# Performance work log

Hardware: AMD Instinct MI355X
Metric: run time of the kernel (lower is better)

## Reference

```python
import jax, jax.numpy as jnp
import numpy as np

DECAY_INIT = 0.9
SPECTRAL_RADIUS = 0.5
EPS = 1e-8


def _spectral_normed(W, u, radius):
    # 3 power iterations (no-grad in torch); u, v treated as constants.
    for _ in range(3):
        v = W.T @ u
        v = v / (jnp.linalg.norm(v) + EPS)
        u = W @ v
        u = u / (jnp.linalg.norm(u) + EPS)
    u = jax.lax.stop_gradient(u)
    v = jax.lax.stop_gradient(v)
    sigma = jnp.abs(u @ W @ v)
    return W * (radius / (sigma + EPS))


def setup_inputs() -> dict:
    key = jax.random.key(0)
    ks = jax.random.split(key, 6)
    T, B, D, n = 2048, 8, 1024, 64
    xavier = float(np.sqrt(2.0 / (D + n)))
    x = jax.random.normal(ks[0], (T, B, D), dtype=jnp.float32)
    S0 = jnp.zeros((B, n, n), dtype=jnp.float32)
    W_k = jax.random.normal(ks[1], (n, D), dtype=jnp.float32) * xavier
    W_v = jax.random.normal(ks[2], (n, D), dtype=jnp.float32) * xavier
    W_q = jax.random.normal(ks[3], (n, D), dtype=jnp.float32) * xavier
    u_k = jax.random.normal(ks[4], (n,), dtype=jnp.float32)
    u_k = u_k / (jnp.linalg.norm(u_k) + EPS)
    u_v = jax.random.normal(ks[5], (n,), dtype=jnp.float32)
    u_v = u_v / (jnp.linalg.norm(u_v) + EPS)
    return {"x": x, "S0": S0, "W_k": W_k, "W_v": W_v, "W_q": W_q,
            "u_k": u_k, "u_v": u_v}


def reference(x, S0, W_k, W_v, W_q, u_k, u_v):
    # decay = clamp(0.9, 0, 0.999).item() -> detached constant
    decay = jnp.clip(jnp.float32(DECAY_INIT), 0.0, 0.999)
    Wk = _spectral_normed(W_k, u_k, SPECTRAL_RADIUS)
    Wv = _spectral_normed(W_v, u_v, SPECTRAL_RADIUS)

    # projections: [T, B, n]
    k_all = jnp.einsum('tbd,nd->tbn', x, Wk)
    v_all = jnp.einsum('tbd,nd->tbn', x, Wv)
    q_all = jnp.einsum('tbd,nd->tbn', x, W_q)

    def step(S, kvq):
        k, v, q = kvq  # each [B, n]
        S = decay * S + v[:, :, None] * k[:, None, :]  # [B, n, n]
        sq = jnp.einsum('bij,bj->bi', S, q)
        out = sq * jax.nn.silu(sq)
        return S, (S, out)

    _, (S_seq, output) = jax.lax.scan(step, S0, (k_all, v_all, q_all))
    S_all = jnp.concatenate([S0[None], S_seq], axis=0)  # [T+1, B, n, n]
    return output, S_all
```

## Files before the change

kernel.cpp:

```cpp
#include <hip/hip_runtime.h>
#include <math.h>

#define T_DIM 2048
#define B_DIM 8
#define D_DIM 1024
#define N_DIM 64
#define NCHUNK 16
#define CHUNK_LEN 128
#define DECAY 0.9f
#define EPS 1e-8f
#define RADIUS 0.5f

typedef __attribute__((ext_vector_type(8))) short short8;
typedef __attribute__((ext_vector_type(4))) float f32x4;

static __device__ __forceinline__ unsigned short f2bf(float f) {
    unsigned u = __float_as_uint(f);
    u += 0x7FFFu + ((u >> 16) & 1u);
    return (unsigned short)(u >> 16);
}
static __device__ __forceinline__ float bf2f(unsigned short h) {
    return __uint_as_float(((unsigned)h) << 16);
}

static __device__ __forceinline__ void bar_lgkm() {
    asm volatile("s_waitcnt lgkmcnt(0)" ::: "memory");
    __builtin_amdgcn_s_barrier();
    asm volatile("" ::: "memory");
}

__global__ __launch_bounds__(256)
void gram_kernel(const float* __restrict__ Wk, const float* __restrict__ Wv,
                 float* __restrict__ G) {
    int mat = blockIdx.x >> 6;
    int i   = blockIdx.x & 63;
    const float* W = mat ? Wv : Wk;
    __shared__ float wsr[D_DIM];
    __shared__ float part[4][64];
    int tid = threadIdx.x;
    *(float4*)&wsr[tid * 4] = *(const float4*)(W + (size_t)i * D_DIM + tid * 4);
    __syncthreads();
    int j = tid & 63, p = tid >> 6;
    const float* wj = W + (size_t)j * D_DIM + p * 256;
    const float* wp = wsr + p * 256;
    float acc = 0.f;
    #pragma unroll 16
    for (int k = 0; k < 256; k += 4) {
        float4 a = *(const float4*)(wj + k);
        float4 b = *(const float4*)(wp + k);
        acc += a.x * b.x + a.y * b.y + a.z * b.z + a.w * b.w;
    }
    part[p][j] = acc;
    __syncthreads();
    if (tid < 64)
        G[((size_t)mat * 64 + i) * 64 + tid] =
            part[0][tid] + part[1][tid] + part[2][tid] + part[3][tid];
}

__global__ __launch_bounds__(256)
void build_wt_kernel(const float* __restrict__ Wk, const float* __restrict__ Wv,
                     const float* __restrict__ Wq, const float* __restrict__ G,
                     const float* __restrict__ uk, const float* __restrict__ uv,
                     unsigned short* __restrict__ BPh, unsigned short* __restrict__ BPl) {
    __shared__ float Gs[64][65];
    __shared__ float us_s[64];
    __shared__ float sc_s;
    int bid = blockIdx.x;
    int g   = bid >> 3;
    int gm  = g >> 2;
    int tid = threadIdx.x;

    if (gm < 2) {
        #pragma unroll
        for (int e = 0; e < 16; ++e) {
            int idx = e * 256 + tid;
            Gs[idx >> 6][idx & 63] = G[(size_t)gm * 4096 + idx];
        }
        if (tid < 64) us_s[tid] = (gm ? uv : uk)[tid];
        __syncthreads();
        if (tid < 64) {
            int i = tid;
            float sigma = 0.f;
            for (int it = 0; it < 3; ++it) {
                float t = 0.f;
                #pragma unroll
                for (int jj = 0; jj < 64; ++jj)
                    t += Gs[i][jj] * us_s[jj];
                float nv2 = us_s[i] * t;
                #pragma unroll
                for (int o = 32; o > 0; o >>= 1) nv2 += __shfl_xor(nv2, o, 64);
                float nv = sqrtf(fmaxf(nv2, 0.f));
                float ur = t / (nv + EPS);
                float nu2 = ur * ur;
                #pragma unroll
                for (int o = 32; o > 0; o >>= 1) nu2 += __shfl_xor(nu2, o, 64);
                float nu = sqrtf(nu2);
                if (it == 2) sigma = nu2 / (nu + EPS);
                us_s[i] = ur / (nu + EPS);
            }
            if (tid == 0) sc_s = RADIUS / (sigma + EPS);
        }
    } else {
        if (tid == 0) sc_s = 1.0f;
    }
    __syncthreads();
    float sc = sc_s;

    const float* W = (gm == 0) ? Wk : (gm == 1) ? Wv : Wq;
    int subb = bid & 7;
    int m    = subb * 256 + tid;
    int s    = m >> 7;
    int kk   = (m >> 6) & 1;
    int flh  = (m >> 4) & 3;
    int fl   = m & 15;
    int row  = (g & 3) * 16 + fl;
    int k0   = s * 64 + kk * 32 + flh * 8;
    const float* src = W + (size_t)row * D_DIM + k0;
    float4 a = *(const float4*)src;
    float4 b = *(const float4*)(src + 4);
    float v[8] = {a.x, a.y, a.z, a.w, b.x, b.y, b.z, b.w};
    short8 hv, lv;
    #pragma unroll
    for (int e = 0; e < 8; ++e) {
        float val = v[e] * sc;
        unsigned short hh = f2bf(val);
        hv[e] = (short)hh;
        lv[e] = (short)f2bf(val - bf2f(hh));
    }
    size_t o = (size_t)g * 16384 + (size_t)m * 8;
    *(short8*)(BPh + o) = hv;
    *(short8*)(BPl + o) = lv;
}

#define PBM 32
#define KSTAGE 128
__global__ __launch_bounds__(256)
void proj_mfma_kernel(const float* __restrict__ x,
                      const unsigned short* __restrict__ BPh,
                      const unsigned short* __restrict__ BPl,
                      float* __restrict__ kvq) {
    __shared__ __align__(16) unsigned short ldsA[2][PBM * KSTAGE];
    int tid = threadIdx.x;
    int lane = tid & 63;
    int wv = tid >> 6;
    int fl15 = lane & 15;
    int flh = lane >> 4;
    int rowBase = blockIdx.x * PBM;

    int r_st = tid >> 3;
    int sub  = tid & 7;
    const float* xrow = x + (size_t)(rowBase + r_st) * D_DIM + sub * 8;
    int wb0 = r_st * 256 + ((sub * 16) ^ ((r_st & 7) << 4));
    int wb1 = wb0 + 128;

    const unsigned short* bbh = BPh + (size_t)(wv * 3) * 16384 + lane * 8;
    const unsigned short* bbl = BPl + (size_t)(wv * 3) * 16384 + lane * 8;

    f32x4 acc[2][3];
    #pragma unroll
    for (int mt = 0; mt < 2; ++mt)
        #pragma unroll
        for (int nt = 0; nt < 3; ++nt) acc[mt][nt] = (f32x4)(0.f);

    {
        float4 c0 = *(const float4*)(xrow);
        float4 c1 = *(const float4*)(xrow + 4);
        float4 c2 = *(const float4*)(xrow + 64);
        float4 c3 = *(const float4*)(xrow + 68);
        float v0[8] = {c0.x, c0.y, c0.z, c0.w, c1.x, c1.y, c1.z, c1.w};
        float v1[8] = {c2.x, c2.y, c2.z, c2.w, c3.x, c3.y, c3.z, c3.w};
        short8 h0, h1;
        #pragma unroll
        for (int e = 0; e < 8; ++e) {
            h0[e] = (short)f2bf(v0[e]);
            h1[e] = (short)f2bf(v1[e]);
        }
        char* pH = (char*)&ldsA[0][0];
        *(short8*)(pH + wb0) = h0;
        *(short8*)(pH + wb1) = h1;
    }
    float4 p0 = *(const float4*)(xrow + KSTAGE);
    float4 p1 = *(const float4*)(xrow + KSTAGE + 4);
    float4 p2 = *(const float4*)(xrow + KSTAGE + 64);
    float4 p3 = *(const float4*)(xrow + KSTAGE + 68);
    bar_lgkm();

    #pragma unroll 1
    for (int qt = 0; qt < 8; ++qt) {
        int buf = qt & 1;
        const char* pH = (const char*)&ldsA[buf][0];
        #pragma unroll
        for (int s = 0; s < 2; ++s) {
            int sg = qt * 2 + s;
            short8 bh[2][3], bl[2][3];
            #pragma unroll
            for (int nt = 0; nt < 3; ++nt)
                #pragma unroll
                for (int kk = 0; kk < 2; ++kk) {
                    size_t off = (size_t)nt * 16384 + sg * 1024 + kk * 512;
                    bh[kk][nt] = *(const short8*)(bbh + off);
                    bl[kk][nt] = *(const short8*)(bbl + off);
                }
            #pragma unroll
            for (int kk = 0; kk < 2; ++kk) {
                short8 ah[2];
                #pragma unroll
                for (int mt = 0; mt < 2; ++mt) {
                    int row = mt * 16 + fl15;
                    int off = row * 256 + s * 128 +
                              ((kk * 64 + flh * 16) ^ ((row & 7) << 4));
                    ah[mt] = *(const short8*)(pH + off);
                }
                #pragma unroll
                for (int mt = 0; mt < 2; ++mt)
                    #pragma unroll
                    for (int nt = 0; nt < 3; ++nt) {
                        acc[mt][nt] = __builtin_amdgcn_mfma_f32_16x16x32_bf16(
                            ah[mt], bh[kk][nt], acc[mt][nt], 0, 0, 0);
                        acc[mt][nt] = __builtin_amdgcn_mfma_f32_16x16x32_bf16(
                            ah[mt], bl[kk][nt], acc[mt][nt], 0, 0, 0);
                    }
            }
        }
        float4 q0, q1, q2, q3;
        if (qt < 6) {
            const float* nx = xrow + (qt + 2) * KSTAGE;
            q0 = *(const float4*)(nx);
            q1 = *(const float4*)(nx + 4);
            q2 = *(const float4*)(nx + 64);
            q3 = *(const float4*)(nx + 68);
        }
        if (qt < 7) {
            float v0[8] = {p0.x, p0.y, p0.z, p0.w, p1.x, p1.y, p1.z, p1.w};
            float v1[8] = {p2.x, p2.y, p2.z, p2.w, p3.x, p3.y, p3.z, p3.w};
            short8 h0, h1;
            #pragma unroll
            for (int e = 0; e < 8; ++e) {
                h0[e] = (short)f2bf(v0[e]);
                h1[e] = (short)f2bf(v1[e]);
            }
            char* qH = (char*)&ldsA[buf ^ 1][0];
            *(short8*)(qH + wb0) = h0;
            *(short8*)(qH + wb1) = h1;
        }
        bar_lgkm();
        p0 = q0; p1 = q1; p2 = q2; p3 = q3;
    }

    #pragma unroll
    for (int mt = 0; mt < 2; ++mt)
        #pragma unroll
        for (int nt = 0; nt < 3; ++nt) {
            int col = wv * 48 + nt * 16 + fl15;
            #pragma unroll
            for (int r = 0; r < 4; ++r) {
                int row = rowBase + mt * 16 + flh * 4 + r;
                kvq[(size_t)row * 192 + col] = acc[mt][nt][r];
            }
        }
}

#define SC_TILE 8
__global__ __launch_bounds__(256)
void scan_kernel(const float* __restrict__ kvq,
                 const float* __restrict__ S0,
                 float* __restrict__ out,
                 float* __restrict__ S_all) {
    __shared__ __align__(16) float P[4][SC_TILE][4][20];
    int widL = threadIdx.x >> 6;
    int lane = threadIdx.x & 63;
    int r  = lane >> 4;
    int jq = lane & 15;
    int blk = blockIdx.x;
    int c  = blk >> 5;
    int b  = (blk >> 2) & 7;
    int ig = blk & 3;
    int i0 = ig * 16 + widL * 4;
    int i  = i0 + r;

    int pp   = lane >> 1;
    int ur   = pp >> 2;
    int rr   = pp & 3;
    int half = lane & 1;

    if (c == 0) {
        f32x4 s0v = *(const f32x4*)&S0[((size_t)b * 64 + i) * 64 + jq * 4];
        *(f32x4*)&S_all[(size_t)b * 4096 + (size_t)i * 64 + jq * 4] = s0v;
    }

    f32x4 s = (f32x4)(0.f);
    if (c > 0) {
        int tp = (c - 1) * CHUNK_LEN;
        #pragma unroll 4
        for (int u = 0; u < CHUNK_LEN; ++u) {
            const float* base = kvq + (size_t)((tp + u) * B_DIM + b) * 192;
            f32x4 k4 = *(const f32x4*)(base + jq * 4);
            float v  = base[64 + i];
            s.x = __builtin_fmaf(DECAY, s.x, v * k4.x);
            s.y = __builtin_fmaf(DECAY, s.y, v * k4.y);
            s.z = __builtin_fmaf(DECAY, s.z, v * k4.z);
            s.w = __builtin_fmaf(DECAY, s.w, v * k4.w);
        }
    }

    int t0 = c * CHUNK_LEN;
    for (int tb = 0; tb < CHUNK_LEN; tb += SC_TILE) {
        #pragma unroll
        for (int u = 0; u < SC_TILE; ++u) {
            int t = t0 + tb + u;
            const float* base = kvq + (size_t)(t * B_DIM + b) * 192;
            f32x4 k4 = *(const f32x4*)(base + jq * 4);
            f32x4 q4 = *(const f32x4*)(base + 128 + jq * 4);
            float v  = base[64 + i];
            s.x = __builtin_fmaf(DECAY, s.x, v * k4.x);
            s.y = __builtin_fmaf(DECAY, s.y, v * k4.y);
            s.z = __builtin_fmaf(DECAY, s.z, v * k4.z);
            s.w = __builtin_fmaf(DECAY, s.w, v * k4.w);
            __builtin_nontemporal_store(
                s, (f32x4*)&S_all[((size_t)(t + 1) * B_DIM + b) * 4096 +
                                  (size_t)i * 64 + jq * 4]);
            P[widL][u][r][jq] = s.x * q4.x + s.y * q4.y + s.z * q4.z + s.w * q4.w;
        }
        const float* pr = &P[widL][ur][rr][half * 8];
        f32x4 a0 = *(const f32x4*)pr;
        f32x4 a1 = *(const f32x4*)(pr + 4);
        float acc = (a0.x + a0.y) + (a0.z + a0.w) + (a1.x + a1.y) + (a1.z + a1.w);
        acc += __shfl_xor(acc, 1, 64);
        if (half == 0) {
            int t = t0 + tb + ur;
            float sg = 1.0f / (1.0f + __expf(-acc));
            out[((size_t)t * B_DIM + b) * 64 + i0 + rr] = acc * acc * sg;
        }
    }
}

extern "C" void kernel_launch(void* const* d_in, const int* in_sizes, int n_in,
                              void* d_out, int out_size, void* d_ws, size_t ws_size,
                              hipStream_t stream) {
    const float* x  = (const float*)d_in[0];
    const float* S0 = (const float*)d_in[1];
    const float* Wk = (const float*)d_in[2];
    const float* Wv = (const float*)d_in[3];
    const float* Wq = (const float*)d_in[4];
    const float* uk = (const float*)d_in[5];
    const float* uv = (const float*)d_in[6];

    float* out   = (float*)d_out;
    float* S_all = out + (size_t)T_DIM * B_DIM * N_DIM;

    float* ws    = (float*)d_ws;
    float* kvq   = ws;
    unsigned short* BPh = (unsigned short*)(kvq + (size_t)16384 * 192);
    unsigned short* BPl = BPh + (size_t)192 * D_DIM;
    float* G      = (float*)(BPl + (size_t)192 * D_DIM);

    gram_kernel<<<128, 256, 0, stream>>>(Wk, Wv, G);
    build_wt_kernel<<<96, 256, 0, stream>>>(Wk, Wv, Wq, G, uk, uv, BPh, BPl);
    proj_mfma_kernel<<<T_DIM * B_DIM / PBM, 256, 0, stream>>>(x, BPh, BPl, kvq);
    scan_kernel<<<NCHUNK * B_DIM * 4, 256, 0, stream>>>(kvq, S0, out, S_all);
}
```

Before: 113.0 us.

## Fuse gram and weight packing, defer spectral-norm scaling into scan kernel

Merges the Gram-matrix and bf16 hi/lo weight-packing kernels into one launch, removing a kernel launch and its dependency gap. The spectral-norm power iteration moves into the scan kernel's prologue, and the two scale factors are folded into v as a single product sk*sv. The projections are now computed from unscaled weights. Every scan block redundantly recomputes the power iteration, which adds prologue latency to the scan. Splitting each weight value into hi/lo bf16 parts before scaling instead of after could change rounding slightly.

After: 115.9 us. 2.5% more time.

```diff
diff --git a/kernel.cpp b/kernel.cpp
--- a/kernel.cpp
+++ b/kernel.cpp
@@ -30,106 +30,51 @@
 }
 
 __global__ __launch_bounds__(256)
-void gram_kernel(const float* __restrict__ Wk, const float* __restrict__ Wv,
-                 float* __restrict__ G) {
+void gram_pack_kernel(const float* __restrict__ Wk, const float* __restrict__ Wv,
+                      const float* __restrict__ Wq, float* __restrict__ G,
+                      unsigned short* __restrict__ BPh, unsigned short* __restrict__ BPl) {
     int mat = blockIdx.x >> 6;
     int i   = blockIdx.x & 63;
-    const float* W = mat ? Wv : Wk;
+    const float* W = (mat == 0) ? Wk : (mat == 1) ? Wv : Wq;
     __shared__ float wsr[D_DIM];
     __shared__ float part[4][64];
     int tid = threadIdx.x;
     *(float4*)&wsr[tid * 4] = *(const float4*)(W + (size_t)i * D_DIM + tid * 4);
     __syncthreads();
-    int j = tid & 63, p = tid >> 6;
-    const float* wj = W + (size_t)j * D_DIM + p * 256;
-    const float* wp = wsr + p * 256;
-    float acc = 0.f;
-    #pragma unroll 16
-    for (int k = 0; k < 256; k += 4) {
-        float4 a = *(const float4*)(wj + k);
-        float4 b = *(const float4*)(wp + k);
-        acc += a.x * b.x + a.y * b.y + a.z * b.z + a.w * b.w;
-    }
-    part[p][j] = acc;
-    __syncthreads();
-    if (tid < 64)
-        G[((size_t)mat * 64 + i) * 64 + tid] =
-            part[0][tid] + part[1][tid] + part[2][tid] + part[3][tid];
-}
-
-__global__ __launch_bounds__(256)
-void build_wt_kernel(const float* __restrict__ Wk, const float* __restrict__ Wv,
-                     const float* __restrict__ Wq, const float* __restrict__ G,
-                     const float* __restrict__ uk, const float* __restrict__ uv,
-                     unsigned short* __restrict__ BPh, unsigned short* __restrict__ BPl) {
-    __shared__ float Gs[64][65];
-    __shared__ float us_s[64];
-    __shared__ float sc_s;
-    int bid = blockIdx.x;
-    int g   = bid >> 3;
-    int gm  = g >> 2;
-    int tid = threadIdx.x;
-
-    if (gm < 2) {
-        #pragma unroll
-        for (int e = 0; e < 16; ++e) {
-            int idx = e * 256 + tid;
-            Gs[idx >> 6][idx & 63] = G[(size_t)gm * 4096 + idx];
-        }
-        if (tid < 64) us_s[tid] = (gm ? uv : uk)[tid];
+    if (mat < 2) {
+        int j = tid & 63, p = tid >> 6;
+        const float* wj = W + (size_t)j * D_DIM + p * 256;
+        const float* wp = wsr + p * 256;
+        float acc = 0.f;
+        #pragma unroll 16
+        for (int k = 0; k < 256; k += 4) {
+            float4 a = *(const float4*)(wj + k);
+            float4 b = *(const float4*)(wp + k);
+            acc += a.x * b.x + a.y * b.y + a.z * b.z + a.w * b.w;
+        }
+        part[p][j] = acc;
         __syncthreads();
-        if (tid < 64) {
-            int i = tid;
-            float sigma = 0.f;
-            for (int it = 0; it < 3; ++it) {
-                float t = 0.f;
-                #pragma unroll
-                for (int jj = 0; jj < 64; ++jj)
-                    t += Gs[i][jj] * us_s[jj];
-                float nv2 = us_s[i] * t;
-                #pragma unroll
-                for (int o = 32; o > 0; o >>= 1) nv2 += __shfl_xor(nv2, o, 64);
-                float nv = sqrtf(fmaxf(nv2, 0.f));
-                float ur = t / (nv + EPS);
-                float nu2 = ur * ur;
-                #pragma unroll
-                for (int o = 32; o > 0; o >>= 1) nu2 += __shfl_xor(nu2, o, 64);
-                float nu = sqrtf(nu2);
-                if (it == 2) sigma = nu2 / (nu + EPS);
-                us_s[i] = ur / (nu + EPS);
-            }
-            if (tid == 0) sc_s = RADIUS / (sigma + EPS);
-        }
-    } else {
-        if (tid == 0) sc_s = 1.0f;
-    }
-    __syncthreads();
-    float sc = sc_s;
-
-    const float* W = (gm == 0) ? Wk : (gm == 1) ? Wv : Wq;
-    int subb = bid & 7;
-    int m    = subb * 256 + tid;
-    int s    = m >> 7;
-    int kk   = (m >> 6) & 1;
-    int flh  = (m >> 4) & 3;
-    int fl   = m & 15;
-    int row  = (g & 3) * 16 + fl;
-    int k0   = s * 64 + kk * 32 + flh * 8;
-    const float* src = W + (size_t)row * D_DIM + k0;
-    float4 a = *(const float4*)src;
-    float4 b = *(const float4*)(src + 4);
-    float v[8] = {a.x, a.y, a.z, a.w, b.x, b.y, b.z, b.w};
-    short8 hv, lv;
+        if (tid < 64)
+            G[((size_t)mat * 64 + i) * 64 + tid] =
+                part[0][tid] + part[1][tid] + part[2][tid] + part[3][tid];
+    }
+    int g  = mat * 4 + (i >> 4);
+    int fl = i & 15;
+    float4 w4 = *(const float4*)&wsr[tid * 4];
+    float vals[4] = {w4.x, w4.y, w4.z, w4.w};
     #pragma unroll
-    for (int e = 0; e < 8; ++e) {
-        float val = v[e] * sc;
-        unsigned short hh = f2bf(val);
-        hv[e] = (short)hh;
-        lv[e] = (short)f2bf(val - bf2f(hh));
-    }
-    size_t o = (size_t)g * 16384 + (size_t)m * 8;
-    *(short8*)(BPh + o) = hv;
-    *(short8*)(BPl + o) = lv;
+    for (int e4 = 0; e4 < 4; ++e4) {
+        int k = tid * 4 + e4;
+        unsigned short h = f2bf(vals[e4]);
+        unsigned short l = f2bf(vals[e4] - bf2f(h));
+        int s   = k >> 6;
+        int kk  = (k >> 5) & 1;
+        int flh = (k >> 3) & 3;
+        int e   = k & 7;
+        size_t idx = (size_t)g * 16384 + s * 1024 + kk * 512 + (flh * 16 + fl) * 8 + e;
+        BPh[idx] = h;
+        BPl[idx] = l;
+    }
 }
 
 #define PBM 32
@@ -264,11 +209,51 @@
 __global__ __launch_bounds__(256)
 void scan_kernel(const float* __restrict__ kvq,
                  const float* __restrict__ S0,
+                 const float* __restrict__ G,
+                 const float* __restrict__ uk, const float* __restrict__ uv,
                  float* __restrict__ out,
                  float* __restrict__ S_all) {
     __shared__ __align__(16) float P[4][SC_TILE][4][20];
-    int widL = threadIdx.x >> 6;
-    int lane = threadIdx.x & 63;
+    __shared__ float Gs[64][65];
+    __shared__ float usw[4][64];
+    int tid  = threadIdx.x;
+    int widL = tid >> 6;
+    int lane = tid & 63;
+
+    float scs[2];
+    #pragma unroll
+    for (int m2 = 0; m2 < 2; ++m2) {
+        __syncthreads();
+        #pragma unroll
+        for (int e = 0; e < 16; ++e) {
+            int idx = e * 256 + tid;
+            Gs[idx >> 6][idx & 63] = G[(size_t)m2 * 4096 + idx];
+        }
+        usw[widL][lane] = (m2 ? uv : uk)[lane];
+        __syncthreads();
+        float sigma = 0.f;
+        for (int it = 0; it < 3; ++it) {
+            float t = 0.f;
+            #pragma unroll
+            for (int jj = 0; jj < 64; ++jj)
+                t += Gs[lane][jj] * usw[widL][jj];
+            float nv2 = usw[widL][lane] * t;
+            #pragma unroll
+            for (int o = 32; o > 0; o >>= 1) nv2 += __shfl_xor(nv2, o, 64);
+            float nv = sqrtf(fmaxf(nv2, 0.f));
+            float ur = t / (nv + EPS);
+            float nu2 = ur * ur;
+            #pragma unroll
+            for (int o = 32; o > 0; o >>= 1) nu2 += __shfl_xor(nu2, o, 64);
+            float nu = sqrtf(nu2);
+            if (it == 2) sigma = nu2 / (nu + EPS);
+            usw[widL][lane] = ur / (nu + EPS);
+        }
+        scs[m2] = RADIUS / (sigma + EPS);
+    }
+    float sckv = scs[0] * scs[1];
+    __syncthreads();
+
     int r  = lane >> 4;
     int jq = lane & 15;
     int blk = blockIdx.x;
@@ -279,7 +264,7 @@
     int i  = i0 + r;
 
     int pp   = lane >> 1;
-    int ur   = pp >> 2;
+    int ur2  = pp >> 2;
     int rr   = pp & 3;
     int half = lane & 1;
 
@@ -295,7 +280,7 @@
         for (int u = 0; u < CHUNK_LEN; ++u) {
             const float* base = kvq + (size_t)((tp + u) * B_DIM + b) * 192;
             f32x4 k4 = *(const f32x4*)(base + jq * 4);
-            float v  = base[64 + i];
+            float v  = base[64 + i] * sckv;
             s.x = __builtin_fmaf(DECAY, s.x, v * k4.x);
             s.y = __builtin_fmaf(DECAY, s.y, v * k4.y);
             s.z = __builtin_fmaf(DECAY, s.z, v * k4.z);
@@ -311,7 +296,7 @@
             const float* base = kvq + (size_t)(t * B_DIM + b) * 192;
             f32x4 k4 = *(const f32x4*)(base + jq * 4);
             f32x4 q4 = *(const f32x4*)(base + 128 + jq * 4);
-            float v  = base[64 + i];
+            float v  = base[64 + i] * sckv;
             s.x = __builtin_fmaf(DECAY, s.x, v * k4.x);
             s.y = __builtin_fmaf(DECAY, s.y, v * k4.y);
             s.z = __builtin_fmaf(DECAY, s.z, v * k4.z);
@@ -321,13 +306,13 @@
                                   (size_t)i * 64 + jq * 4]);
             P[widL][u][r][jq] = s.x * q4.x + s.y * q4.y + s.z * q4.z + s.w * q4.w;
         }
-        const float* pr = &P[widL][ur][rr][half * 8];
+        const float* pr = &P[widL][ur2][rr][half * 8];
         f32x4 a0 = *(const f32x4*)pr;
         f32x4 a1 = *(const f32x4*)(pr + 4);
         float acc = (a0.x + a0.y) + (a0.z + a0.w) + (a1.x + a1.y) + (a1.z + a1.w);
         acc += __shfl_xor(acc, 1, 64);
         if (half == 0) {
-            int t = t0 + tb + ur;
+            int t = t0 + tb + ur2;
             float sg = 1.0f / (1.0f + __expf(-acc));
             out[((size_t)t * B_DIM + b) * 64 + i0 + rr] = acc * acc * sg;
         }
@@ -354,8 +339,7 @@
     unsigned short* BPl = BPh + (size_t)192 * D_DIM;
     float* G      = (float*)(BPl + (size_t)192 * D_DIM);
 
-    gram_kernel<<<128, 256, 0, stream>>>(Wk, Wv, G);
-    build_wt_kernel<<<96, 256, 0, stream>>>(Wk, Wv, Wq, G, uk, uv, BPh, BPl);
+    gram_pack_kernel<<<192, 256, 0, stream>>>(Wk, Wv, Wq, G, BPh, BPl);
     proj_mfma_kernel<<<T_DIM * B_DIM / PBM, 256, 0, stream>>>(x, BPh, BPl, kvq);
-    scan_kernel<<<NCHUNK * B_DIM * 4, 256, 0, stream>>>(kvq, S0, out, S_all);
-}
+    scan_kernel<<<NCHUNK * B_DIM * 4, 256, 0, stream>>>(kvq, S0, G, uk, uv, out, S_all);
+}
```
